# Optimization experiments

Measured on AMD Instinct MI355X. Metric: run time of the kernel, lower is better.

Reference implementation:

```python
import jax, jax.numpy as jnp
import numpy as np

HID = 512


def _lstm_cell(x, h, c, W_ih, W_hh, b):
    # torch gate order: i, f, g, o ; z: [B, 4H]
    z = x @ W_ih.T + h @ W_hh.T + b
    i, f, g, o = jnp.split(z, 4, axis=-1)
    c_new = jax.nn.sigmoid(f) * c + jax.nn.sigmoid(i) * jnp.tanh(g)
    h_new = jax.nn.sigmoid(o) * jnp.tanh(c_new)
    return h_new, c_new


def setup_inputs() -> dict:
    key = jax.random.key(0)
    ks = jax.random.split(key, 10)
    s = 1.0 / np.sqrt(HID)  # torch default LSTM init scale
    return {
        "inputs": jax.random.normal(ks[0], (512, 512, 1), jnp.float32),
        "targets": jax.random.normal(ks[1], (512, 128, 1), jnp.float32),
        "enc_Wih": jax.random.uniform(ks[2], (4 * HID, 1), jnp.float32, -s, s),
        "enc_Whh": jax.random.uniform(ks[3], (4 * HID, HID), jnp.float32, -s, s),
        "enc_b": jax.random.uniform(ks[4], (4 * HID,), jnp.float32, -s, s),
        "dec_Wih": jax.random.uniform(ks[5], (4 * HID, 1), jnp.float32, -s, s),
        "dec_Whh": jax.random.uniform(ks[6], (4 * HID, HID), jnp.float32, -s, s),
        "dec_b": jax.random.uniform(ks[7], (4 * HID,), jnp.float32, -s, s),
        "lin_W": jax.random.uniform(ks[8], (1, HID), jnp.float32, -s, s),
        "lin_b": jax.random.uniform(ks[9], (1,), jnp.float32, -s, s),
        "target_len": 128,
        "teacher_forcing_ratio": 0,
    }


def reference(inputs, targets, enc_Wih, enc_Whh, enc_b,
              dec_Wih, dec_Whh, dec_b, lin_W, lin_b,
              target_len, teacher_forcing_ratio):
    B = inputs.shape[0]
    H = enc_Whh.shape[1]
    h0 = jnp.zeros((B, H), inputs.dtype)
    c0 = jnp.zeros((B, H), inputs.dtype)

    # ---- encoder: scan over source timesteps ----
    def enc_step(carry, x_t):  # x_t: [B, 1]
        h, c = carry
        h, c = _lstm_cell(x_t, h, c, enc_Wih, enc_Whh, enc_b)
        return (h, c), None

    (h, c), _ = jax.lax.scan(enc_step, (h0, c0), jnp.swapaxes(inputs, 0, 1))

    x0 = inputs[:, -1, :]  # [B, 1]

    def dec_step(carry, _):
        h, c, x = carry
        h, c = _lstm_cell(x, h, c, dec_Wih, dec_Whh, dec_b)
        out = h @ lin_W.T + lin_b  # [B, 1]
        return (h, c, out), out

    _, outs = jax.lax.scan(dec_step, (h, c, x0), None, length=target_len)
    return jnp.swapaxes(outs, 0, 1)  # [B, target_len, 1]
```

## Files before the change

kernel.cpp:

```cpp
#include <hip/hip_runtime.h>
#include <math.h>

#define HID    512
#define BATCH  512
#define TIN    512
#define TOUT   128
#define FOUR_H 2048
#define STEPS  (TIN + TOUT)

typedef __bf16 bf16x8 __attribute__((ext_vector_type(8)));
typedef float floatx4 __attribute__((ext_vector_type(4)));
typedef int   int4v   __attribute__((ext_vector_type(4)));

#define GLOADX4_SC(dst, p) \
    asm volatile("global_load_dwordx4 %0, %1, off sc0 sc1" : "=v"(dst) : "v"(p))
#define GSTOREX4_SC(p, v) \
    asm volatile("global_store_dwordx4 %0, %1, off sc0 sc1" :: "v"(p), "v"(v) : "memory")
#define GLOADX4_C(dst, p) \
    asm volatile("global_load_dwordx4 %0, %1, off" : "=v"(dst) : "v"(p))
#define WAIT_T1(N, r) asm volatile("s_waitcnt vmcnt(" #N ")" : "+v"(r))
#define WAIT_T4(N, B) asm volatile("s_waitcnt vmcnt(" #N ")" \
    : "+v"((B)[0]), "+v"((B)[1]), "+v"((B)[2]), "+v"((B)[3]))

__device__ __forceinline__ float fsig(float x) {
    return __builtin_amdgcn_rcpf(1.0f + __expf(-x));
}
__device__ __forceinline__ float ftanh(float x) {
    return 1.0f - 2.0f * __builtin_amdgcn_rcpf(1.0f + __expf(2.0f * x));
}

__global__ __launch_bounds__(256) void pack_w(
    const float* __restrict__ W, __bf16* __restrict__ Apk)
{
    int tid = blockIdx.x * 256 + threadIdx.x;
    int mp  = tid >> 6;
    int kg  = tid & 63;
    int g   = mp & 3;
    int j   = mp >> 2;
    int r   = g * HID + j;
    int blk   = mp >> 7;
    int rg    = (mp >> 4) & 7;
    int lr    = mp & 15;
    int chunk = kg >> 2;
    int lq    = kg & 3;
    int lane  = lq * 16 + lr;
    const float* src = W + (size_t)r * HID + kg * 8;
    size_t offHi = ((size_t)(((blk * 8 + rg) * 16 + chunk) * 2 + 0) * 512) + lane * 8;
    size_t offLo = ((size_t)(((blk * 8 + rg) * 16 + chunk) * 2 + 1) * 512) + lane * 8;
    __bf16 hibuf[8], lobuf[8];
    #pragma unroll
    for (int i = 0; i < 8; ++i) {
        float x = src[i];
        __bf16 hi = (__bf16)x;
        hibuf[i] = hi;
        lobuf[i] = (__bf16)(x - (float)hi);
    }
    *(bf16x8*)(Apk + offHi) = *(bf16x8*)hibuf;
    *(bf16x8*)(Apk + offLo) = *(bf16x8*)lobuf;
}

__global__ __launch_bounds__(256) void pack_v(
    const float* __restrict__ Wih, const float* __restrict__ b,
    float* __restrict__ WihP, float* __restrict__ bP)
{
    int mp = blockIdx.x * 256 + threadIdx.x;
    int g  = mp & 3;
    int j  = mp >> 2;
    int r  = g * HID + j;
    WihP[mp] = Wih[r];
    bP[mp]   = b[r];
}

__global__ __launch_bounds__(256) void transpose_in(
    const float* __restrict__ in, float* __restrict__ outT)
{
    int idx = blockIdx.x * 256 + threadIdx.x;
    int t = idx >> 9, b = idx & 511;
    outT[idx] = in[(size_t)b * TIN + t];
}

__global__ __launch_bounds__(256, 1) void lstm_persistent(
    const __bf16* __restrict__ ApkEnc,
    const __bf16* __restrict__ ApkDec,
    const float* __restrict__ WihPenc, const float* __restrict__ biasPenc,
    const float* __restrict__ WihPdec, const float* __restrict__ biasPdec,
    const float* __restrict__ inputsT,
    const float* __restrict__ linW, const float* __restrict__ linb,
    __bf16* __restrict__ h0,
    __bf16* __restrict__ h1,
    float* __restrict__ xacc,
    int* __restrict__ barrier_ws,
    float* __restrict__ out)
{
    extern __shared__ char smem[];
    __bf16* Alds   = (__bf16*)smem;
    char*   Bring  = smem + 131072;
    __bf16* hstage = (__bf16*)(smem + 147456);
    float*  xred   = (float*)(smem + 152576);

    const int tid  = threadIdx.x;
    const int lane = tid & 63;
    const int w    = tid >> 6;
    const int lr   = lane & 15;
    const int lq   = lane >> 4;
    const int by   = blockIdx.x >> 4;
    const int blk  = blockIdx.x & 15;
    const int nbase = by * 32;
    const int rgbase = 2 * w;
    const bool STREAM = (w >= 2);

    const int m0a = blk * 128 + (rgbase + 0) * 16 + lq * 4;
    const int m0b = blk * 128 + (rgbase + 1) * 16 + lq * 4;
    const floatx4 wihE[2] = { *(const floatx4*)(WihPenc + m0a), *(const floatx4*)(WihPenc + m0b) };
    const floatx4 bE[2]   = { *(const floatx4*)(biasPenc + m0a), *(const floatx4*)(biasPenc + m0b) };
    const floatx4 wihD[2] = { *(const floatx4*)(WihPdec + m0a), *(const floatx4*)(WihPdec + m0b) };
    const floatx4 bD[2]   = { *(const floatx4*)(biasPdec + m0a), *(const floatx4*)(biasPdec + m0b) };
    const float lw[2] = { linW[m0a >> 2], linW[m0b >> 2] };
    const float lb = linb[0];

    int bn[2];
    #pragma unroll
    for (int nt = 0; nt < 2; ++nt) bn[nt] = nbase + nt * 16 + lr;

    {
        float* hz = (float*)hstage;
        for (int i = tid; i < 1280; i += 256) hz[i] = 0.f;
    }
    {
        const int4v* srcp = (const int4v*)(ApkEnc + (size_t)blk * 131072);
        int4v* dstp = (int4v*)Alds;
        for (int i = tid; i < 8192; i += 256) dstp[i] = srcp[i];
    }
    __syncthreads();

    float creg[2][2] = {{0.f, 0.f}, {0.f, 0.f}};

    int* arrive = barrier_ws + by * 32;
    int* phase  = barrier_ws + 512 + by * 32;

    for (int s = 0; s < STEPS; ++s) {
        const bool dec = (s >= TIN);
        const int  t   = s - TIN;
        const __bf16* Acur = dec ? ApkDec : ApkEnc;

        if (s == TIN) {
            const int4v* srcp = (const int4v*)(ApkDec + (size_t)blk * 131072);
            int4v* dstp = (int4v*)Alds;
            for (int i = tid; i < 8192; i += 256) dstp[i] = srcp[i];
            __syncthreads();
        }

        const __bf16* hin  = (s & 1) ? h1 : h0;
        __bf16*       hout = (s & 1) ? h0 : h1;
        const __bf16* srcB = hin + (size_t)by * 32768 + tid * 8;
        const __bf16* Ag   = Acur + (size_t)blk * 131072;

        float xq[2];
        if (dec) {
            if (tid < 32) xred[tid] = 0.f;
            if (blk == 0) {
                if (t >= 1 && tid < 32) {
                    float v = __hip_atomic_load(&xacc[((t - 1) % 3) * BATCH + nbase + tid],
                                                __ATOMIC_RELAXED, __HIP_MEMORY_SCOPE_AGENT) + lb;
                    out[(size_t)(nbase + tid) * TOUT + (t - 1)] = v;
                }
                if (tid >= 32 && tid < 64) {
                    __hip_atomic_store(&xacc[((t + 1) % 3) * BATCH + nbase + (tid - 32)], 0.0f,
                                       __ATOMIC_RELAXED, __HIP_MEMORY_SCOPE_AGENT);
                }
            }
            #pragma unroll
            for (int nt = 0; nt < 2; ++nt)
                xq[nt] = (t == 0) ? inputsT[(TIN - 1) * BATCH + bn[nt]]
                                  : __hip_atomic_load(&xacc[((t - 1) % 3) * BATCH + bn[nt]],
                                                      __ATOMIC_RELAXED, __HIP_MEMORY_SCOPE_AGENT) + lb;
        } else {
            #pragma unroll
            for (int nt = 0; nt < 2; ++nt)
                xq[nt] = inputsT[s * BATCH + bn[nt]];
        }
        asm volatile("" ::: "memory");

        int4v st[4];
        int4v areg[2][4];
        GLOADX4_SC(st[1], srcB + (size_t)((blk + 1) & 15) * 2048);
        GLOADX4_SC(st[2], srcB + (size_t)((blk + 2) & 15) * 2048);
        if (STREAM) {
            #pragma unroll
            for (int mb = 0; mb < 2; ++mb)
                #pragma unroll
                for (int pl = 0; pl < 2; ++pl)
                    GLOADX4_C(areg[0][mb * 2 + pl],
                              Ag + (size_t)((((rgbase + mb) * 16 + blk) * 2 + pl) * 512) + lane * 8);
        }

        floatx4 acc[2][2];
        #pragma unroll
        for (int mb = 0; mb < 2; ++mb)
            #pragma unroll
            for (int nt = 0; nt < 2; ++nt) acc[mb][nt] = floatx4{0.f, 0.f, 0.f, 0.f};

        #pragma unroll
        for (int it = 0; it < 16; ++it) {
            const int c = (blk + it) & 15;

            if (it > 0) {
                if (STREAM) {
                    if      (it == 1 || it == 14) { WAIT_T1(5, st[it & 3]); }
                    else if (it <= 13)            { WAIT_T1(6, st[it & 3]); }
                    else                          { WAIT_T1(4, st[it & 3]); }
                } else {
                    if      (it <= 13) { WAIT_T1(2, st[it & 3]); }
                    else if (it == 14) { WAIT_T1(1, st[it & 3]); }
                    else               { WAIT_T1(0, st[it & 3]); }
                }
                *(int4v*)(Bring + (it & 3) * 4096 + tid * 16) = st[it & 3];
            }

            if (STREAM && it + 1 < 16) {
                const int cn = (blk + it + 1) & 15;
                #pragma unroll
                for (int mb = 0; mb < 2; ++mb)
                    #pragma unroll
                    for (int pl = 0; pl < 2; ++pl)
                        GLOADX4_C(areg[(it + 1) & 1][mb * 2 + pl],
                                  Ag + (size_t)((((rgbase + mb) * 16 + cn) * 2 + pl) * 512) + lane * 8);
            }
            if (it + 3 < 16)
                GLOADX4_SC(st[(it + 3) & 3], srcB + (size_t)((blk + it + 3) & 15) * 2048);

            if (it > 0) __syncthreads();

            bf16x8 ah[2], al[2];
            if (STREAM) {
                if      (it == 0)  { WAIT_T4(5, areg[0]); }
                else if (it <= 12) { WAIT_T4(6, areg[it & 1]); }
                else if (it == 13) { WAIT_T4(5, areg[1]); }
                else if (it == 14) { WAIT_T4(4, areg[0]); }
                else               { WAIT_T4(0, areg[1]); }
                #pragma unroll
                for (int mb = 0; mb < 2; ++mb) {
                    ah[mb] = __builtin_bit_cast(bf16x8, areg[it & 1][mb * 2 + 0]);
                    al[mb] = __builtin_bit_cast(bf16x8, areg[it & 1][mb * 2 + 1]);
                }
            } else {
                #pragma unroll
                for (int mb = 0; mb < 2; ++mb) {
                    const char* ap = (const char*)Alds
                        + (((rgbase + mb) * 16 + c) * 2) * 1024 + lane * 16;
                    ah[mb] = *(const bf16x8*)(ap);
                    al[mb] = *(const bf16x8*)(ap + 1024);
                }
            }

            bf16x8 bh0, bl0, bh1, bl1;
            if (it == 0) {
                const char* hb = (const char*)hstage;
                const int kq = lane >> 4, lrp = lane & 15;
                bh0 = *(const bf16x8*)(hb + (     lrp) * 80 + kq * 16);
                bl0 = *(const bf16x8*)(hb + (32 + lrp) * 80 + kq * 16);
                bh1 = *(const bf16x8*)(hb + (16 + lrp) * 80 + kq * 16);
                bl1 = *(const bf16x8*)(hb + (48 + lrp) * 80 + kq * 16);
            } else {
                const char* bs = Bring + (it & 3) * 4096;
                bh0 = *(const bf16x8*)(bs + (0 * 128 + 0 * 64 + lane) * 16);
                bl0 = *(const bf16x8*)(bs + (0 * 128 + 1 * 64 + lane) * 16);
                bh1 = *(const bf16x8*)(bs + (1 * 128 + 0 * 64 + lane) * 16);
                bl1 = *(const bf16x8*)(bs + (1 * 128 + 1 * 64 + lane) * 16);
            }

            #pragma unroll
            for (int mb = 0; mb < 2; ++mb) {
                acc[mb][0] = __builtin_amdgcn_mfma_f32_16x16x32_bf16(ah[mb], bh0, acc[mb][0], 0, 0, 0);
                acc[mb][1] = __builtin_amdgcn_mfma_f32_16x16x32_bf16(ah[mb], bh1, acc[mb][1], 0, 0, 0);
                acc[mb][0] = __builtin_amdgcn_mfma_f32_16x16x32_bf16(al[mb], bh0, acc[mb][0], 0, 0, 0);
                acc[mb][1] = __builtin_amdgcn_mfma_f32_16x16x32_bf16(al[mb], bh1, acc[mb][1], 0, 0, 0);
                acc[mb][0] = __builtin_amdgcn_mfma_f32_16x16x32_bf16(ah[mb], bl0, acc[mb][0], 0, 0, 0);
                acc[mb][1] = __builtin_amdgcn_mfma_f32_16x16x32_bf16(ah[mb], bl1, acc[mb][1], 0, 0, 0);
            }
        }

        const floatx4* wih = dec ? wihD : wihE;
        const floatx4* bb  = dec ? bD   : bE;
        float px[2] = {0.f, 0.f};
        #pragma unroll
        for (int mb = 0; mb < 2; ++mb) {
            const int jlocal = (rgbase + mb) * 4 + lq;
            #pragma unroll
            for (int nt = 0; nt < 2; ++nt) {
                float x  = xq[nt];
                float i_ = fsig (acc[mb][nt][0] + bb[mb][0] + x * wih[mb][0]);
                float f_ = fsig (acc[mb][nt][1] + bb[mb][1] + x * wih[mb][1]);
                float g_ = ftanh(acc[mb][nt][2] + bb[mb][2] + x * wih[mb][2]);
                float o_ = fsig (acc[mb][nt][3] + bb[mb][3] + x * wih[mb][3]);
                float cv = f_ * creg[mb][nt] + i_ * g_;
                creg[mb][nt] = cv;
                float h  = o_ * ftanh(cv);
                __bf16 hh = (__bf16)h;
                int bl = nt * 16 + lr;
                hstage[bl * 40 + jlocal] = hh;
                hstage[(32 + bl) * 40 + jlocal] = (__bf16)(h - (float)hh);
                if (dec) {
                    float v = h * lw[mb];
                    px[nt] += v;
                }
            }
        }
        if (dec) {
            #pragma unroll
            for (int nt = 0; nt < 2; ++nt) {
                px[nt] += __shfl_xor(px[nt], 16);
                px[nt] += __shfl_xor(px[nt], 32);
            }
        }

        __syncthreads();

        {
            int nt = tid >> 7, pl = (tid >> 6) & 1, ln = tid & 63;
            int kq = ln >> 4, lrp = ln & 15;
            const char* src = (const char*)hstage + (pl * 32 + nt * 16 + lrp) * 80 + kq * 16;
            int4v v = *(const int4v*)src;
            __bf16* dst = hout + (size_t)by * 32768 + blk * 2048 + tid * 8;
            GSTOREX4_SC(dst, v);
        }

        if (dec && lane < 16) {
            #pragma unroll
            for (int nt = 0; nt < 2; ++nt) atomicAdd(&xred[nt * 16 + lr], px[nt]);
        }
        __syncthreads();
        if (dec && tid < 32) {
            atomicAdd(&xacc[(t % 3) * BATCH + nbase + tid], xred[tid]);
        }

        __builtin_amdgcn_s_waitcnt(0);
        __syncthreads();
        if (tid == 0) {
            int n = __hip_atomic_fetch_add(arrive, 1, __ATOMIC_RELAXED, __HIP_MEMORY_SCOPE_AGENT);
            if (n == 16 * (s + 1) - 1) {
                __hip_atomic_store(phase, s + 1, __ATOMIC_RELAXED, __HIP_MEMORY_SCOPE_AGENT);
            } else {
                int p;
                do {
                    __builtin_amdgcn_s_sleep(2);
                    p = __hip_atomic_load(phase, __ATOMIC_RELAXED, __HIP_MEMORY_SCOPE_AGENT);
                } while (p < s + 1);
            }
        }
        __syncthreads();
    }

    if (blk == 0 && tid < 32) {
        float v = __hip_atomic_load(&xacc[((TOUT - 1) % 3) * BATCH + nbase + tid],
                                    __ATOMIC_RELAXED, __HIP_MEMORY_SCOPE_AGENT) + lb;
        out[(size_t)(nbase + tid) * TOUT + (TOUT - 1)] = v;
    }
}

extern "C" void kernel_launch(void* const* d_in, const int* in_sizes, int n_in,
                              void* d_out, int out_size, void* d_ws, size_t ws_size,
                              hipStream_t stream) {
    const float* inputs  = (const float*)d_in[0];
    const float* enc_Wih = (const float*)d_in[2];
    const float* enc_Whh = (const float*)d_in[3];
    const float* enc_b   = (const float*)d_in[4];
    const float* dec_Wih = (const float*)d_in[5];
    const float* dec_Whh = (const float*)d_in[6];
    const float* dec_b   = (const float*)d_in[7];
    const float* lin_W   = (const float*)d_in[8];
    const float* lin_b   = (const float*)d_in[9];
    float* out = (float*)d_out;

    char* ws = (char*)d_ws;
    const size_t SZ_APK = (size_t)FOUR_H * HID * 2 * sizeof(__bf16);
    const size_t SZ_V   = (size_t)FOUR_H * sizeof(float);
    const size_t SZ_HF  = (size_t)16 * 16 * 256 * 8 * sizeof(__bf16);

    __bf16* ApkEnc = (__bf16*)(ws);
    __bf16* ApkDec = (__bf16*)(ws + SZ_APK);
    char* p = ws + 2 * SZ_APK;
    float* WihPenc  = (float*)p;  p += SZ_V;
    float* biasPenc = (float*)p;  p += SZ_V;
    float* WihPdec  = (float*)p;  p += SZ_V;
    float* biasPdec = (float*)p;  p += SZ_V;
    float* inputsT  = (float*)p;  p += (size_t)TIN * BATCH * sizeof(float);
    __bf16* h0 = (__bf16*)p;      p += SZ_HF;
    __bf16* h1 = (__bf16*)p;      p += SZ_HF;
    float* xacc  = (float*)p;     p += 3 * BATCH * sizeof(float);
    int* barrier_ws = (int*)p;    p += 1024 * sizeof(int);

    pack_w<<<512, 256, 0, stream>>>(enc_Whh, ApkEnc);
    pack_w<<<512, 256, 0, stream>>>(dec_Whh, ApkDec);
    pack_v<<<8, 256, 0, stream>>>(enc_Wih, enc_b, WihPenc, biasPenc);
    pack_v<<<8, 256, 0, stream>>>(dec_Wih, dec_b, WihPdec, biasPdec);
    transpose_in<<<1024, 256, 0, stream>>>(inputs, inputsT);
    hipMemsetAsync(h0, 0, SZ_HF, stream);
    hipMemsetAsync(xacc, 0, 3 * BATCH * sizeof(float), stream);
    hipMemsetAsync(barrier_ws, 0, 1024 * sizeof(int), stream);

    const int shmem = 131072 + 16384 + 5120 + 128;
    hipFuncSetAttribute((const void*)lstm_persistent,
                        hipFuncAttributeMaxDynamicSharedMemorySize, shmem);

    void* args[] = {
        (void*)&ApkEnc, (void*)&ApkDec,
        (void*)&WihPenc, (void*)&biasPenc, (void*)&WihPdec, (void*)&biasPdec,
        (void*)&inputsT, (void*)&lin_W, (void*)&lin_b,
        (void*)&h0, (void*)&h1,
        (void*)&xacc, (void*)&barrier_ws, (void*)&out
    };
    hipLaunchCooperativeKernel((void*)lstm_persistent, dim3(256), dim3(256),
                               args, shmem, stream);
}
```

Baseline: 4.426 ms.

## Replace group barrier with per-block flags and triple-buffer hidden state

Replaces the counter-plus-phase group barrier with per-block step flags that each consumer polls before reading peers' hidden state. The hidden state becomes triple-buffered so a fast block can write the next step without overwriting data a slower peer still reads. The local-chunk MFMA work (from the block's own staged h) is moved ahead of the wait, overlapping the barrier latency with compute and prefetching two A tiles early. This loosens synchronization to point-to-point dependencies at the cost of polling sixteen flags per step and one more hidden-state buffer.

```diff
diff --git a/kernel.cpp b/kernel.cpp
--- a/kernel.cpp
+++ b/kernel.cpp
@@ -88,6 +88,7 @@
     const float* __restrict__ linW, const float* __restrict__ linb,
     __bf16* __restrict__ h0,
     __bf16* __restrict__ h1,
+    __bf16* __restrict__ h2,
     float* __restrict__ xacc,
     int* __restrict__ barrier_ws,
     float* __restrict__ out)
@@ -109,6 +110,8 @@
     const int rgbase = 2 * w;
     const bool STREAM = (w >= 2);
 
+    int* flagv = barrier_ws;
+
     const int m0a = blk * 128 + (rgbase + 0) * 16 + lq * 4;
     const int m0b = blk * 128 + (rgbase + 1) * 16 + lq * 4;
     const floatx4 wihE[2] = { *(const floatx4*)(WihPenc + m0a), *(const floatx4*)(WihPenc + m0b) };
@@ -135,8 +138,9 @@
 
     float creg[2][2] = {{0.f, 0.f}, {0.f, 0.f}};
 
-    int* arrive = barrier_ws + by * 32;
-    int* phase  = barrier_ws + 512 + by * 32;
+    __bf16* hA = h0;
+    __bf16* hB = h1;
+    __bf16* hC = h2;
 
     for (int s = 0; s < STEPS; ++s) {
         const bool dec = (s >= TIN);
@@ -150,12 +154,85 @@
             __syncthreads();
         }
 
-        const __bf16* hin  = (s & 1) ? h1 : h0;
-        __bf16*       hout = (s & 1) ? h0 : h1;
-        const __bf16* srcB = hin + (size_t)by * 32768 + tid * 8;
+        const __bf16* srcB = hA + (size_t)by * 32768 + tid * 8;
+        __bf16*       hout = hB;
         const __bf16* Ag   = Acur + (size_t)blk * 131072;
 
         float xq[2];
+        if (!dec) {
+            #pragma unroll
+            for (int nt = 0; nt < 2; ++nt)
+                xq[nt] = inputsT[s * BATCH + bn[nt]];
+            asm volatile("" ::: "memory");
+        }
+
+        int4v st[4];
+        int4v areg[2][4];
+        if (STREAM) {
+            #pragma unroll
+            for (int mb = 0; mb < 2; ++mb)
+                #pragma unroll
+                for (int pl = 0; pl < 2; ++pl)
+                    GLOADX4_C(areg[0][mb * 2 + pl],
+                              Ag + (size_t)((((rgbase + mb) * 16 + blk) * 2 + pl) * 512) + lane * 8);
+            #pragma unroll
+            for (int mb = 0; mb < 2; ++mb)
+                #pragma unroll
+                for (int pl = 0; pl < 2; ++pl)
+                    GLOADX4_C(areg[1][mb * 2 + pl],
+                              Ag + (size_t)((((rgbase + mb) * 16 + ((blk + 1) & 15)) * 2 + pl) * 512) + lane * 8);
+        }
+
+        if (tid < 16) {
+            const int* fp = &flagv[by * 16 + tid];
+            while (__hip_atomic_load(fp, __ATOMIC_RELAXED, __HIP_MEMORY_SCOPE_AGENT) < s) {
+                __builtin_amdgcn_s_sleep(1);
+            }
+        }
+
+        floatx4 acc[2][2];
+        #pragma unroll
+        for (int mb = 0; mb < 2; ++mb)
+            #pragma unroll
+            for (int nt = 0; nt < 2; ++nt) acc[mb][nt] = floatx4{0.f, 0.f, 0.f, 0.f};
+
+        {
+            bf16x8 ah[2], al[2];
+            if (STREAM) {
+                WAIT_T4(4, areg[0]);
+                #pragma unroll
+                for (int mb = 0; mb < 2; ++mb) {
+                    ah[mb] = __builtin_bit_cast(bf16x8, areg[0][mb * 2 + 0]);
+                    al[mb] = __builtin_bit_cast(bf16x8, areg[0][mb * 2 + 1]);
+                }
+            } else {
+                #pragma unroll
+                for (int mb = 0; mb < 2; ++mb) {
+                    const char* ap = (const char*)Alds
+                        + (((rgbase + mb) * 16 + blk) * 2) * 1024 + lane * 16;
+                    ah[mb] = *(const bf16x8*)(ap);
+                    al[mb] = *(const bf16x8*)(ap + 1024);
+                }
+            }
+            const char* hb = (const char*)hstage;
+            const int kq = lane >> 4, lrp = lane & 15;
+            bf16x8 bh0 = *(const bf16x8*)(hb + (     lrp) * 80 + kq * 16);
+            bf16x8 bl0 = *(const bf16x8*)(hb + (32 + lrp) * 80 + kq * 16);
+            bf16x8 bh1 = *(const bf16x8*)(hb + (16 + lrp) * 80 + kq * 16);
+            bf16x8 bl1 = *(const bf16x8*)(hb + (48 + lrp) * 80 + kq * 16);
+            #pragma unroll
+            for (int mb = 0; mb < 2; ++mb) {
+                acc[mb][0] = __builtin_amdgcn_mfma_f32_16x16x32_bf16(ah[mb], bh0, acc[mb][0], 0, 0, 0);
+                acc[mb][1] = __builtin_amdgcn_mfma_f32_16x16x32_bf16(ah[mb], bh1, acc[mb][1], 0, 0, 0);
+                acc[mb][0] = __builtin_amdgcn_mfma_f32_16x16x32_bf16(al[mb], bh0, acc[mb][0], 0, 0, 0);
+                acc[mb][1] = __builtin_amdgcn_mfma_f32_16x16x32_bf16(al[mb], bh1, acc[mb][1], 0, 0, 0);
+                acc[mb][0] = __builtin_amdgcn_mfma_f32_16x16x32_bf16(ah[mb], bl0, acc[mb][0], 0, 0, 0);
+                acc[mb][1] = __builtin_amdgcn_mfma_f32_16x16x32_bf16(ah[mb], bl1, acc[mb][1], 0, 0, 0);
+            }
+        }
+
+        __syncthreads();
+
         if (dec) {
             if (tid < 32) xred[tid] = 0.f;
             if (blk == 0) {
@@ -174,48 +251,29 @@
                 xq[nt] = (t == 0) ? inputsT[(TIN - 1) * BATCH + bn[nt]]
                                   : __hip_atomic_load(&xacc[((t - 1) % 3) * BATCH + bn[nt]],
                                                       __ATOMIC_RELAXED, __HIP_MEMORY_SCOPE_AGENT) + lb;
-        } else {
-            #pragma unroll
-            for (int nt = 0; nt < 2; ++nt)
-                xq[nt] = inputsT[s * BATCH + bn[nt]];
-        }
-        asm volatile("" ::: "memory");
-
-        int4v st[4];
-        int4v areg[2][4];
+            asm volatile("" ::: "memory");
+        }
+
         GLOADX4_SC(st[1], srcB + (size_t)((blk + 1) & 15) * 2048);
         GLOADX4_SC(st[2], srcB + (size_t)((blk + 2) & 15) * 2048);
-        if (STREAM) {
-            #pragma unroll
-            for (int mb = 0; mb < 2; ++mb)
-                #pragma unroll
-                for (int pl = 0; pl < 2; ++pl)
-                    GLOADX4_C(areg[0][mb * 2 + pl],
-                              Ag + (size_t)((((rgbase + mb) * 16 + blk) * 2 + pl) * 512) + lane * 8);
-        }
-
-        floatx4 acc[2][2];
+        GLOADX4_SC(st[3], srcB + (size_t)((blk + 3) & 15) * 2048);
+
         #pragma unroll
-        for (int mb = 0; mb < 2; ++mb)
-            #pragma unroll
-            for (int nt = 0; nt < 2; ++nt) acc[mb][nt] = floatx4{0.f, 0.f, 0.f, 0.f};
-
-        #pragma unroll
-        for (int it = 0; it < 16; ++it) {
+        for (int it = 1; it < 16; ++it) {
             const int c = (blk + it) & 15;
 
-            if (it > 0) {
-                if (STREAM) {
-                    if      (it == 1 || it == 14) { WAIT_T1(5, st[it & 3]); }
-                    else if (it <= 13)            { WAIT_T1(6, st[it & 3]); }
-                    else                          { WAIT_T1(4, st[it & 3]); }
-                } else {
-                    if      (it <= 13) { WAIT_T1(2, st[it & 3]); }
-                    else if (it == 14) { WAIT_T1(1, st[it & 3]); }
-                    else               { WAIT_T1(0, st[it & 3]); }
-                }
-                *(int4v*)(Bring + (it & 3) * 4096 + tid * 16) = st[it & 3];
-            }
+            if (STREAM) {
+                if      (it == 1)  { WAIT_T1(2,  st[it & 3]); }
+                else if (it == 2)  { WAIT_T1(6,  st[it & 3]); }
+                else if (it <= 13) { WAIT_T1(10, st[it & 3]); }
+                else if (it == 14) { WAIT_T1(9,  st[it & 3]); }
+                else               { WAIT_T1(8,  st[it & 3]); }
+            } else {
+                if      (it <= 13) { WAIT_T1(2, st[it & 3]); }
+                else if (it == 14) { WAIT_T1(1, st[it & 3]); }
+                else               { WAIT_T1(0, st[it & 3]); }
+            }
+            *(int4v*)(Bring + (it & 3) * 4096 + tid * 16) = st[it & 3];
 
             if (STREAM && it + 1 < 16) {
                 const int cn = (blk + it + 1) & 15;
@@ -229,11 +287,11 @@
             if (it + 3 < 16)
                 GLOADX4_SC(st[(it + 3) & 3], srcB + (size_t)((blk + it + 3) & 15) * 2048);
 
-            if (it > 0) __syncthreads();
+            __syncthreads();
 
             bf16x8 ah[2], al[2];
             if (STREAM) {
-                if      (it == 0)  { WAIT_T4(5, areg[0]); }
+                if      (it == 1)  { WAIT_T4(7, areg[1]); }
                 else if (it <= 12) { WAIT_T4(6, areg[it & 1]); }
                 else if (it == 13) { WAIT_T4(5, areg[1]); }
                 else if (it == 14) { WAIT_T4(4, areg[0]); }
@@ -253,21 +311,11 @@
                 }
             }
 
-            bf16x8 bh0, bl0, bh1, bl1;
-            if (it == 0) {
-                const char* hb = (const char*)hstage;
-                const int kq = lane >> 4, lrp = lane & 15;
-                bh0 = *(const bf16x8*)(hb + (     lrp) * 80 + kq * 16);
-                bl0 = *(const bf16x8*)(hb + (32 + lrp) * 80 + kq * 16);
-                bh1 = *(const bf16x8*)(hb + (16 + lrp) * 80 + kq * 16);
-                bl1 = *(const bf16x8*)(hb + (48 + lrp) * 80 + kq * 16);
-            } else {
-                const char* bs = Bring + (it & 3) * 4096;
-                bh0 = *(const bf16x8*)(bs + (0 * 128 + 0 * 64 + lane) * 16);
-                bl0 = *(const bf16x8*)(bs + (0 * 128 + 1 * 64 + lane) * 16);
-                bh1 = *(const bf16x8*)(bs + (1 * 128 + 0 * 64 + lane) * 16);
-                bl1 = *(const bf16x8*)(bs + (1 * 128 + 1 * 64 + lane) * 16);
-            }
+            const char* bs = Bring + (it & 3) * 4096;
+            bf16x8 bh0 = *(const bf16x8*)(bs + (0 * 128 + 0 * 64 + lane) * 16);
+            bf16x8 bl0 = *(const bf16x8*)(bs + (0 * 128 + 1 * 64 + lane) * 16);
+            bf16x8 bh1 = *(const bf16x8*)(bs + (1 * 128 + 0 * 64 + lane) * 16);
+            bf16x8 bl1 = *(const bf16x8*)(bs + (1 * 128 + 1 * 64 + lane) * 16);
 
             #pragma unroll
             for (int mb = 0; mb < 2; ++mb) {
@@ -337,24 +385,26 @@
         __builtin_amdgcn_s_waitcnt(0);
         __syncthreads();
         if (tid == 0) {
-            int n = __hip_atomic_fetch_add(arrive, 1, __ATOMIC_RELAXED, __HIP_MEMORY_SCOPE_AGENT);
-            if (n == 16 * (s + 1) - 1) {
-                __hip_atomic_store(phase, s + 1, __ATOMIC_RELAXED, __HIP_MEMORY_SCOPE_AGENT);
-            } else {
-                int p;
-                do {
-                    __builtin_amdgcn_s_sleep(2);
-                    p = __hip_atomic_load(phase, __ATOMIC_RELAXED, __HIP_MEMORY_SCOPE_AGENT);
-                } while (p < s + 1);
+            __hip_atomic_store(&flagv[by * 16 + blk], s + 1,
+                               __ATOMIC_RELAXED, __HIP_MEMORY_SCOPE_AGENT);
+        }
+
+        __bf16* htmp = hA; hA = hB; hB = hC; hC = htmp;
+    }
+
+    if (blk == 0) {
+        if (tid < 16) {
+            const int* fp = &flagv[by * 16 + tid];
+            while (__hip_atomic_load(fp, __ATOMIC_RELAXED, __HIP_MEMORY_SCOPE_AGENT) < STEPS) {
+                __builtin_amdgcn_s_sleep(1);
             }
         }
         __syncthreads();
-    }
-
-    if (blk == 0 && tid < 32) {
-        float v = __hip_atomic_load(&xacc[((TOUT - 1) % 3) * BATCH + nbase + tid],
-                                    __ATOMIC_RELAXED, __HIP_MEMORY_SCOPE_AGENT) + lb;
-        out[(size_t)(nbase + tid) * TOUT + (TOUT - 1)] = v;
+        if (tid < 32) {
+            float v = __hip_atomic_load(&xacc[((TOUT - 1) % 3) * BATCH + nbase + tid],
+                                        __ATOMIC_RELAXED, __HIP_MEMORY_SCOPE_AGENT) + lb;
+            out[(size_t)(nbase + tid) * TOUT + (TOUT - 1)] = v;
+        }
     }
 }
 
@@ -387,6 +437,7 @@
     float* inputsT  = (float*)p;  p += (size_t)TIN * BATCH * sizeof(float);
     __bf16* h0 = (__bf16*)p;      p += SZ_HF;
     __bf16* h1 = (__bf16*)p;      p += SZ_HF;
+    __bf16* h2 = (__bf16*)p;      p += SZ_HF;
     float* xacc  = (float*)p;     p += 3 * BATCH * sizeof(float);
     int* barrier_ws = (int*)p;    p += 1024 * sizeof(int);
 
@@ -407,7 +458,7 @@
         (void*)&ApkEnc, (void*)&ApkDec,
         (void*)&WihPenc, (void*)&biasPenc, (void*)&WihPdec, (void*)&biasPdec,
         (void*)&inputsT, (void*)&lin_W, (void*)&lin_b,
-        (void*)&h0, (void*)&h1,
+        (void*)&h0, (void*)&h1, (void*)&h2,
         (void*)&xacc, (void*)&barrier_ws, (void*)&out
     };
     hipLaunchCooperativeKernel((void*)lstm_persistent, dim3(256), dim3(256),
```

After: 5.013 ms. 1.13x slower.

## Replace group barrier with per-block step flags and triple-buffered hidden state

Applied to the files above, without the earlier changes.

Each of the 16 blocks in a batch group used to meet at an arrive/phase counter barrier after every timestep. Now each block publishes a per-block step flag. At the start of the next step it polls the 16 flags of its group, skipping the poll when a flag prefetched at the end of the previous step already shows the others have arrived. The hidden state moves from double to triple buffering, so a fast block can write step s+1 while slower blocks still read step s. This removes the serialized atomic counter and lets blocks drift by up to one step, at the cost of an extra buffer and more subtle ordering that depends on relaxed atomics and the xacc ring.

```diff
diff --git a/kernel.cpp b/kernel.cpp
--- a/kernel.cpp
+++ b/kernel.cpp
@@ -88,6 +88,7 @@
     const float* __restrict__ linW, const float* __restrict__ linb,
     __bf16* __restrict__ h0,
     __bf16* __restrict__ h1,
+    __bf16* __restrict__ h2,
     float* __restrict__ xacc,
     int* __restrict__ barrier_ws,
     float* __restrict__ out)
@@ -109,6 +110,8 @@
     const int rgbase = 2 * w;
     const bool STREAM = (w >= 2);
 
+    int* flagv = barrier_ws;
+
     const int m0a = blk * 128 + (rgbase + 0) * 16 + lq * 4;
     const int m0b = blk * 128 + (rgbase + 1) * 16 + lq * 4;
     const floatx4 wihE[2] = { *(const floatx4*)(WihPenc + m0a), *(const floatx4*)(WihPenc + m0b) };
@@ -135,8 +138,11 @@
 
     float creg[2][2] = {{0.f, 0.f}, {0.f, 0.f}};
 
-    int* arrive = barrier_ws + by * 32;
-    int* phase  = barrier_ws + 512 + by * 32;
+    __bf16* hA = h0;
+    __bf16* hB = h1;
+    __bf16* hC = h2;
+
+    int fpref = 0;
 
     for (int s = 0; s < STEPS; ++s) {
         const bool dec = (s >= TIN);
@@ -150,9 +156,19 @@
             __syncthreads();
         }
 
-        const __bf16* hin  = (s & 1) ? h1 : h0;
-        __bf16*       hout = (s & 1) ? h0 : h1;
-        const __bf16* srcB = hin + (size_t)by * 32768 + tid * 8;
+        {
+            bool lag = (lane < 16) && (fpref < s);
+            if (__ballot(lag) != 0ULL) {
+                if (lane < 16) {
+                    const int* fp = &flagv[by * 16 + lane];
+                    while (__hip_atomic_load(fp, __ATOMIC_RELAXED, __HIP_MEMORY_SCOPE_AGENT) < s)
+                        __builtin_amdgcn_s_sleep(2);
+                }
+            }
+        }
+
+        const __bf16* srcB = hA + (size_t)by * 32768 + tid * 8;
+        __bf16*       hout = hB;
         const __bf16* Ag   = Acur + (size_t)blk * 131072;
 
         float xq[2];
@@ -337,24 +353,30 @@
         __builtin_amdgcn_s_waitcnt(0);
         __syncthreads();
         if (tid == 0) {
-            int n = __hip_atomic_fetch_add(arrive, 1, __ATOMIC_RELAXED, __HIP_MEMORY_SCOPE_AGENT);
-            if (n == 16 * (s + 1) - 1) {
-                __hip_atomic_store(phase, s + 1, __ATOMIC_RELAXED, __HIP_MEMORY_SCOPE_AGENT);
-            } else {
-                int p;
-                do {
-                    __builtin_amdgcn_s_sleep(2);
-                    p = __hip_atomic_load(phase, __ATOMIC_RELAXED, __HIP_MEMORY_SCOPE_AGENT);
-                } while (p < s + 1);
+            __hip_atomic_store(&flagv[by * 16 + blk], s + 1,
+                               __ATOMIC_RELAXED, __HIP_MEMORY_SCOPE_AGENT);
+        }
+        if (lane < 16) {
+            fpref = __hip_atomic_load(&flagv[by * 16 + lane],
+                                      __ATOMIC_RELAXED, __HIP_MEMORY_SCOPE_AGENT);
+        }
+
+        __bf16* htmp = hA; hA = hB; hB = hC; hC = htmp;
+    }
+
+    if (blk == 0) {
+        if (tid < 16) {
+            const int* fp = &flagv[by * 16 + tid];
+            while (__hip_atomic_load(fp, __ATOMIC_RELAXED, __HIP_MEMORY_SCOPE_AGENT) < STEPS) {
+                __builtin_amdgcn_s_sleep(2);
             }
         }
         __syncthreads();
-    }
-
-    if (blk == 0 && tid < 32) {
-        float v = __hip_atomic_load(&xacc[((TOUT - 1) % 3) * BATCH + nbase + tid],
-                                    __ATOMIC_RELAXED, __HIP_MEMORY_SCOPE_AGENT) + lb;
-        out[(size_t)(nbase + tid) * TOUT + (TOUT - 1)] = v;
+        if (tid < 32) {
+            float v = __hip_atomic_load(&xacc[((TOUT - 1) % 3) * BATCH + nbase + tid],
+                                        __ATOMIC_RELAXED, __HIP_MEMORY_SCOPE_AGENT) + lb;
+            out[(size_t)(nbase + tid) * TOUT + (TOUT - 1)] = v;
+        }
     }
 }
 
@@ -387,6 +409,7 @@
     float* inputsT  = (float*)p;  p += (size_t)TIN * BATCH * sizeof(float);
     __bf16* h0 = (__bf16*)p;      p += SZ_HF;
     __bf16* h1 = (__bf16*)p;      p += SZ_HF;
+    __bf16* h2 = (__bf16*)p;      p += SZ_HF;
     float* xacc  = (float*)p;     p += 3 * BATCH * sizeof(float);
     int* barrier_ws = (int*)p;    p += 1024 * sizeof(int);
 
@@ -407,7 +430,7 @@
         (void*)&ApkEnc, (void*)&ApkDec,
         (void*)&WihPenc, (void*)&biasPenc, (void*)&WihPdec, (void*)&biasPdec,
         (void*)&inputsT, (void*)&lin_W, (void*)&lin_b,
-        (void*)&h0, (void*)&h1,
+        (void*)&h0, (void*)&h1, (void*)&h2,
         (void*)&xacc, (void*)&barrier_ws, (void*)&out
     };
     hipLaunchCooperativeKernel((void*)lstm_persistent, dim3(256), dim3(256),
```

Result: slower. 4.988 ms (+12.7%).

## Remap blocks by XCC so each batch group shares an L2, relax cache bypass

Applied to the files above, without the earlier changes.

At kernel start each workgroup reads its XCC id from a hardware register, counts how many workgroups sit on each XCC after a global handshake, and takes a logical slot so the 16 blocks sharing a batch group (by) land on the same XCC. The hidden-state loads and stores then drop the sc1 bit and use sc0 only, so the h exchange can go through the shared per-XCC L2 instead of bypassing to memory. This aims to cut the per-step latency of the h exchange. It relies on each batch group's blocks really being co-resident on one XCC (32 per XCC); if the layout is uneven, groups span XCCs and the L2-scoped traffic may not be coherent. It also adds a one-time startup barrier.

```diff
diff --git a/kernel.cpp b/kernel.cpp
--- a/kernel.cpp
+++ b/kernel.cpp
@@ -12,10 +12,10 @@
 typedef float floatx4 __attribute__((ext_vector_type(4)));
 typedef int   int4v   __attribute__((ext_vector_type(4)));
 
-#define GLOADX4_SC(dst, p) \
-    asm volatile("global_load_dwordx4 %0, %1, off sc0 sc1" : "=v"(dst) : "v"(p))
-#define GSTOREX4_SC(p, v) \
-    asm volatile("global_store_dwordx4 %0, %1, off sc0 sc1" :: "v"(p), "v"(v) : "memory")
+#define GLOADX4_L2(dst, p) \
+    asm volatile("global_load_dwordx4 %0, %1, off sc0" : "=v"(dst) : "v"(p))
+#define GSTOREX4_L2(p, v) \
+    asm volatile("global_store_dwordx4 %0, %1, off sc0" :: "v"(p), "v"(v) : "memory")
 #define GLOADX4_C(dst, p) \
     asm volatile("global_load_dwordx4 %0, %1, off" : "=v"(dst) : "v"(p))
 #define WAIT_T1(N, r) asm volatile("s_waitcnt vmcnt(" #N ")" : "+v"(r))
@@ -97,14 +97,35 @@
     char*   Bring  = smem + 131072;
     __bf16* hstage = (__bf16*)(smem + 147456);
     float*  xred   = (float*)(smem + 152576);
+    __shared__ int sh_gslot;
 
     const int tid  = threadIdx.x;
     const int lane = tid & 63;
     const int w    = tid >> 6;
     const int lr   = lane & 15;
     const int lq   = lane >> 4;
-    const int by   = blockIdx.x >> 4;
-    const int blk  = blockIdx.x & 15;
+
+    if (tid == 0) {
+        unsigned xcc = __builtin_amdgcn_s_getreg((31u << 11) | 20u) & 7u;
+        __hip_atomic_fetch_add(&barrier_ws[1024 + (int)xcc], 1,
+                               __ATOMIC_RELAXED, __HIP_MEMORY_SCOPE_AGENT);
+        __hip_atomic_fetch_add(&barrier_ws[1032], 1,
+                               __ATOMIC_RELEASE, __HIP_MEMORY_SCOPE_AGENT);
+        while (__hip_atomic_load(&barrier_ws[1032],
+                                 __ATOMIC_ACQUIRE, __HIP_MEMORY_SCOPE_AGENT) < 256)
+            __builtin_amdgcn_s_sleep(2);
+        int pre = 0;
+        for (int x = 0; x < (int)xcc; ++x)
+            pre += __hip_atomic_load(&barrier_ws[1024 + x],
+                                     __ATOMIC_RELAXED, __HIP_MEMORY_SCOPE_AGENT);
+        int slot = __hip_atomic_fetch_add(&barrier_ws[1040 + (int)xcc], 1,
+                                          __ATOMIC_RELAXED, __HIP_MEMORY_SCOPE_AGENT);
+        sh_gslot = pre + slot;
+    }
+    __syncthreads();
+    const int gslot = sh_gslot;
+    const int by  = gslot >> 4;
+    const int blk = gslot & 15;
     const int nbase = by * 32;
     const int rgbase = 2 * w;
     const bool STREAM = (w >= 2);
@@ -183,8 +204,8 @@
 
         int4v st[4];
         int4v areg[2][4];
-        GLOADX4_SC(st[1], srcB + (size_t)((blk + 1) & 15) * 2048);
-        GLOADX4_SC(st[2], srcB + (size_t)((blk + 2) & 15) * 2048);
+        GLOADX4_L2(st[1], srcB + (size_t)((blk + 1) & 15) * 2048);
+        GLOADX4_L2(st[2], srcB + (size_t)((blk + 2) & 15) * 2048);
         if (STREAM) {
             #pragma unroll
             for (int mb = 0; mb < 2; ++mb)
@@ -227,7 +248,7 @@
                                   Ag + (size_t)((((rgbase + mb) * 16 + cn) * 2 + pl) * 512) + lane * 8);
             }
             if (it + 3 < 16)
-                GLOADX4_SC(st[(it + 3) & 3], srcB + (size_t)((blk + it + 3) & 15) * 2048);
+                GLOADX4_L2(st[(it + 3) & 3], srcB + (size_t)((blk + it + 3) & 15) * 2048);
 
             if (it > 0) __syncthreads();
 
@@ -322,7 +343,7 @@
             const char* src = (const char*)hstage + (pl * 32 + nt * 16 + lrp) * 80 + kq * 16;
             int4v v = *(const int4v*)src;
             __bf16* dst = hout + (size_t)by * 32768 + blk * 2048 + tid * 8;
-            GSTOREX4_SC(dst, v);
+            GSTOREX4_L2(dst, v);
         }
 
         if (dec && lane < 16) {
@@ -388,7 +409,7 @@
     __bf16* h0 = (__bf16*)p;      p += SZ_HF;
     __bf16* h1 = (__bf16*)p;      p += SZ_HF;
     float* xacc  = (float*)p;     p += 3 * BATCH * sizeof(float);
-    int* barrier_ws = (int*)p;    p += 1024 * sizeof(int);
+    int* barrier_ws = (int*)p;    p += 1056 * sizeof(int);
 
     pack_w<<<512, 256, 0, stream>>>(enc_Whh, ApkEnc);
     pack_w<<<512, 256, 0, stream>>>(dec_Whh, ApkDec);
@@ -397,7 +418,7 @@
     transpose_in<<<1024, 256, 0, stream>>>(inputs, inputsT);
     hipMemsetAsync(h0, 0, SZ_HF, stream);
     hipMemsetAsync(xacc, 0, 3 * BATCH * sizeof(float), stream);
-    hipMemsetAsync(barrier_ws, 0, 1024 * sizeof(int), stream);
+    hipMemsetAsync(barrier_ws, 0, 1056 * sizeof(int), stream);
 
     const int shmem = 131072 + 16384 + 5120 + 128;
     hipFuncSetAttribute((const void*)lstm_persistent,
```

Result: slower. 9.512 ms (+114.9%).
